# Optimization experiments

Hardware: AMD Instinct MI355X
Metric: run time of the kernel (lower is better)

Reference implementation:

```python
import jax, jax.numpy as jnp
import numpy as np

EPS = 1e-6

def _phi(u):
    # positive feature map used by linear attention
    return jax.nn.elu(u) + 1.0

def setup_inputs() -> dict:
    key = jax.random.key(0)
    ks = jax.random.split(key, 5)
    B, T, D = 8, 2048, 512  # batch, seq_len, d_model == in_features == out_features
    scale = 1.0 / np.sqrt(D)
    x = jax.random.normal(ks[0], (B, T, D), dtype=jnp.float32)
    Wq = (jax.random.normal(ks[1], (D, D), dtype=jnp.float32) * scale)
    Wk = (jax.random.normal(ks[2], (D, D), dtype=jnp.float32) * scale)
    Wv = (jax.random.normal(ks[3], (D, D), dtype=jnp.float32) * scale)
    Wp = (jax.random.normal(ks[4], (D, D), dtype=jnp.float32) * scale)  # output projection (bias=False)
    return {"x": x, "Wq": Wq, "Wk": Wk, "Wv": Wv, "Wp": Wp}

def reference(x, Wq, Wk, Wv, Wp):
    # x: [B, T, D]
    B, T, D = x.shape
    q = _phi(x @ Wq)  # [B, T, D]
    k = _phi(x @ Wk)  # [B, T, D]
    v = x @ Wv        # [B, T, D]

    # recurrent linear-attention cell, stepped over time via lax.scan
    def step(carry, qkv):
        S, z = carry              # S: [B, D, D] running sum of k^T v; z: [B, D] running sum of k
        qt, kt, vt = qkv          # each [B, D]
        S = S + kt[:, :, None] * vt[:, None, :]
        z = z + kt
        num = jnp.einsum('bd,bde->be', qt, S)        # [B, D]
        den = jnp.einsum('bd,bd->b', qt, z) + EPS    # [B]
        return (S, z), num / den[:, None]

    qT = jnp.swapaxes(q, 0, 1)  # [T, B, D]
    kT = jnp.swapaxes(k, 0, 1)
    vT = jnp.swapaxes(v, 0, 1)
    init = (jnp.zeros((B, D, D), dtype=x.dtype), jnp.zeros((B, D), dtype=x.dtype))
    _, yT = jax.lax.scan(step, init, (qT, kT, vT))  # yT: [T, B, D]
    y = jnp.swapaxes(yT, 0, 1)                      # [B, T, D]
    return y @ Wp                                   # final bias-free projection
```

## Files before the change

kernel.cpp:

```cpp
#include <hip/hip_runtime.h>


typedef __attribute__((ext_vector_type(4))) float f32x4;
typedef __attribute__((ext_vector_type(8))) __bf16 bf16x8;
typedef __attribute__((ext_vector_type(8))) unsigned short ushort8;

constexpr size_t OFF_XB  = 0;
constexpr size_t OFF_WT  = OFF_XB + 16777216;
constexpr size_t OFF_Q   = OFF_WT + 2097152;
constexpr size_t OFF_KK  = OFF_Q  + 16777216;
constexpr size_t OFF_KT  = OFF_KK + 16777216;
constexpr size_t OFF_VT  = OFF_KT + 16777216;
constexpr size_t OFF_G   = OFF_VT + 16777216;
constexpr size_t OFF_MT  = OFF_G  + 8388608;
constexpr size_t OFF_Y   = OFF_MT + 33554432;
constexpr size_t OFF_ZP  = OFF_Y  + 16777216;
constexpr size_t OFF_DEN = OFF_ZP + 131072;
constexpr size_t WS_NEED = OFF_DEN + 65536;

__device__ __forceinline__ unsigned short bfbits(float f) {
  __bf16 h = (__bf16)f;
  return __builtin_bit_cast(unsigned short, h);
}
__device__ __forceinline__ float bff(unsigned short u) {
  return (float)__builtin_bit_cast(__bf16, u);
}

__device__ __forceinline__ void gload16(const void* g, void* l) {
  __builtin_amdgcn_global_load_lds((const __attribute__((address_space(1))) void*)g,
                                   (__attribute__((address_space(3))) void*)l, 16, 0, 0);
}

__device__ __forceinline__ void stage_half(const char* gRow0, size_t ld2, int k0b,
                                           char* ldsHalf, int w, int lane) {
#pragma unroll
  for (int i = 0; i < 2; ++i) {
    int L = (w << 10) + (lane << 4) + (i << 13);
    int r = L >> 7;
    int cb = (L & 127) ^ ((r & 7) << 4);
    gload16(gRow0 + (size_t)r * ld2 + k0b + cb, ldsHalf + (w << 10) + (i << 13));
  }
}

__device__ __forceinline__ const bf16x8* frag_at(const char* halfBase, int rowInHalf,
                                                 int colByte) {
  int lin = (rowInHalf << 7) + colByte;
  lin ^= (rowInHalf & 7) << 4;
  return (const bf16x8*)(halfBase + lin);
}

#define QUAD(mh, nh)                                                                   \
  _Pragma("unroll") for (int mm = 0; mm < 4; ++mm)                                     \
  _Pragma("unroll") for (int nn = 0; nn < 2; ++nn)                                     \
  _Pragma("unroll") for (int s = 0; s < 2; ++s)                                        \
      acc[(mh)*4 + mm][(nh)*2 + nn] = __builtin_amdgcn_mfma_f32_16x16x32_bf16(         \
          af[(mh)*4 + mm][s], bg[(nh)*2 + nn][s], acc[(mh)*4 + mm][(nh)*2 + nn], 0, 0, 0);

#define PHASE_TAIL(MH, NH)                                       \
  __builtin_amdgcn_s_barrier();                                  \
  asm volatile("s_waitcnt lgkmcnt(0)" ::: "memory");             \
  __builtin_amdgcn_sched_barrier(0);                             \
  __builtin_amdgcn_s_setprio(1);                                 \
  QUAD(MH, NH);                                                  \
  __builtin_amdgcn_s_setprio(0);                                 \
  __builtin_amdgcn_s_barrier();

__device__ __forceinline__ void core8(const char* Ab, size_t lda2, const char* Bb,
                                      size_t ldb2, int nt, char* sA, char* sB,
                                      f32x4 (&acc)[8][4], int w, int lane) {
  const int mr = w >> 2, nc = w & 3;
  const int fr = lane & 15, foB = (lane >> 4) << 4;
  const int brow = (nc & 1) << 6;
  const char* gA0 = Ab;
  const char* gA1 = Ab + (size_t)128 * lda2;
  const char* gB0 = Bb;
  const char* gB1 = Bb + (size_t)128 * ldb2;
  bf16x8 af[8][2], bg[4][2];

  stage_half(gA0, lda2, 0, sA + 0 * 16384, w, lane);
  stage_half(gA1, lda2, 0, sA + 1 * 16384, w, lane);
  stage_half(gB0, ldb2, 0, sB + 0 * 16384, w, lane);
  stage_half(gB1, ldb2, 0, sB + 1 * 16384, w, lane);
  if (nt > 1) {
    stage_half(gA0, lda2, 128, sA + 2 * 16384, w, lane);
    stage_half(gA1, lda2, 128, sA + 3 * 16384, w, lane);
    asm volatile("s_waitcnt vmcnt(4)" ::: "memory");
  } else {
    asm volatile("s_waitcnt vmcnt(0)" ::: "memory");
  }
  __builtin_amdgcn_sched_barrier(0);
  __builtin_amdgcn_s_barrier();

  for (int t = 0; t < nt; ++t) {
    const int buf = t & 1;
    const char* cA = sA + buf * 32768 + mr * 16384;
    const char* cB = sB + buf * 32768 + (nc >> 1) * 16384;
    char* nA = sA + buf * 32768;
    char* nB = sB + (buf ^ 1) * 32768;
    const int kb1 = (t + 1) << 7, kb2 = (t + 2) << 7;
    const bool stB = (t + 1 < nt), stA = (t + 2 < nt);

#pragma unroll
    for (int m = 0; m < 4; ++m)
#pragma unroll
      for (int s = 0; s < 2; ++s) af[m][s] = *frag_at(cA, m * 16 + fr, s * 64 + foB);
#pragma unroll
    for (int n = 0; n < 2; ++n)
#pragma unroll
      for (int s = 0; s < 2; ++s)
        bg[n][s] = *frag_at(cB, brow + n * 16 + fr, s * 64 + foB);
    if (stB) stage_half(gB0, ldb2, kb1, nB + 0 * 16384, w, lane);
    PHASE_TAIL(0, 0)

#pragma unroll
    for (int m = 4; m < 8; ++m)
#pragma unroll
      for (int s = 0; s < 2; ++s) af[m][s] = *frag_at(cA, m * 16 + fr, s * 64 + foB);
    if (stB) stage_half(gB1, ldb2, kb1, nB + 1 * 16384, w, lane);
    PHASE_TAIL(1, 0)

#pragma unroll
    for (int n = 2; n < 4; ++n)
#pragma unroll
      for (int s = 0; s < 2; ++s)
        bg[n][s] = *frag_at(cB, brow + n * 16 + fr, s * 64 + foB);
    if (stA) stage_half(gA0, lda2, kb2, nA + 0 * 16384, w, lane);
    PHASE_TAIL(0, 1)

    if (stA) stage_half(gA1, lda2, kb2, nA + 1 * 16384, w, lane);
    if (t < nt - 2) {
      asm volatile("s_waitcnt vmcnt(4)" ::: "memory");
      __builtin_amdgcn_sched_barrier(0);
    } else if (t == nt - 2) {
      asm volatile("s_waitcnt vmcnt(0)" ::: "memory");
      __builtin_amdgcn_sched_barrier(0);
    }
    PHASE_TAIL(1, 1)
  }
}

#define QUADH(mh, nh)                                                                  \
  _Pragma("unroll") for (int mm = 0; mm < 2; ++mm)                                     \
  _Pragma("unroll") for (int nn = 0; nn < 2; ++nn)                                     \
  _Pragma("unroll") for (int s = 0; s < 2; ++s)                                        \
      acc[(mh)*2 + mm][(nh)*2 + nn] = __builtin_amdgcn_mfma_f32_16x16x32_bf16(         \
          af[(mh)*2 + mm][s], bg[(nh)*2 + nn][s], acc[(mh)*2 + mm][(nh)*2 + nn], 0, 0, 0);

#define PHASE_TAILH(MH, NH)                                      \
  __builtin_amdgcn_s_barrier();                                  \
  asm volatile("s_waitcnt lgkmcnt(0)" ::: "memory");             \
  __builtin_amdgcn_sched_barrier(0);                             \
  __builtin_amdgcn_s_setprio(1);                                 \
  QUADH(MH, NH);                                                 \
  __builtin_amdgcn_s_setprio(0);                                 \
  __builtin_amdgcn_s_barrier();

__device__ __forceinline__ void core8h(const char* Ab, size_t lda2, const char* Bb,
                                       size_t ldb2, int nt, char* sA, char* sB,
                                       f32x4 (&acc)[4][4], int w, int lane) {
  const int wr = w >> 2, wc = w & 3;
  const int fr = lane & 15, foB = (lane >> 4) << 4;
  const int brow = (wc & 1) << 6;
  const char* gB1 = Bb + (size_t)128 * ldb2;
  bf16x8 af[4][2], bg[4][2];

  stage_half(Ab, lda2, 0, sA + 0, w, lane);
  stage_half(Bb, ldb2, 0, sB + 0, w, lane);
  stage_half(gB1, ldb2, 0, sB + 16384, w, lane);
  if (nt > 1) {
    stage_half(Ab, lda2, 128, sA + 16384, w, lane);
    asm volatile("s_waitcnt vmcnt(2)" ::: "memory");
  } else {
    asm volatile("s_waitcnt vmcnt(0)" ::: "memory");
  }
  __builtin_amdgcn_sched_barrier(0);
  __builtin_amdgcn_s_barrier();

  for (int t = 0; t < nt; ++t) {
    const int buf = t & 1;
    const char* cA = sA + buf * 16384;
    const char* cB = sB + buf * 32768 + (wc >> 1) * 16384;
    char* nA = sA + buf * 16384;
    char* nB = sB + (buf ^ 1) * 32768;
    const int kb1 = (t + 1) << 7, kb2 = (t + 2) << 7;
    const bool stB = (t + 1 < nt), stA = (t + 2 < nt);

#pragma unroll
    for (int m = 0; m < 2; ++m)
#pragma unroll
      for (int s = 0; s < 2; ++s)
        af[m][s] = *frag_at(cA, wr * 64 + m * 16 + fr, s * 64 + foB);
#pragma unroll
    for (int n = 0; n < 2; ++n)
#pragma unroll
      for (int s = 0; s < 2; ++s)
        bg[n][s] = *frag_at(cB, brow + n * 16 + fr, s * 64 + foB);
    if (stB) stage_half(Bb, ldb2, kb1, nB + 0, w, lane);
    PHASE_TAILH(0, 0)

#pragma unroll
    for (int m = 2; m < 4; ++m)
#pragma unroll
      for (int s = 0; s < 2; ++s)
        af[m][s] = *frag_at(cA, wr * 64 + m * 16 + fr, s * 64 + foB);
    if (stB) stage_half(gB1, ldb2, kb1, nB + 16384, w, lane);
    PHASE_TAILH(1, 0)

#pragma unroll
    for (int n = 2; n < 4; ++n)
#pragma unroll
      for (int s = 0; s < 2; ++s)
        bg[n][s] = *frag_at(cB, brow + n * 16 + fr, s * 64 + foB);
    if (stA) stage_half(Ab, lda2, kb2, nA, w, lane);
    PHASE_TAILH(0, 1)

    if (t < nt - 1) {
      if (stA) {
        asm volatile("s_waitcnt vmcnt(2)" ::: "memory");
      } else {
        asm volatile("s_waitcnt vmcnt(0)" ::: "memory");
      }
      __builtin_amdgcn_sched_barrier(0);
    }
    PHASE_TAILH(1, 1)
  }
}

#define ACC8_INIT                                    \
  f32x4 acc[8][4];                                   \
  _Pragma("unroll") for (int m_ = 0; m_ < 8; ++m_)   \
  _Pragma("unroll") for (int n_ = 0; n_ < 4; ++n_)   \
      acc[m_][n_] = f32x4{0.f, 0.f, 0.f, 0.f};

#define ACC4_INIT                                    \
  f32x4 acc[4][4];                                   \
  _Pragma("unroll") for (int m_ = 0; m_ < 4; ++m_)   \
  _Pragma("unroll") for (int n_ = 0; n_ < 4; ++n_)   \
      acc[m_][n_] = f32x4{0.f, 0.f, 0.f, 0.f};

__global__ __launch_bounds__(512, 2) void k8_qkvt(const ushort* __restrict__ xb,
                                                  const ushort* __restrict__ wt,
                                                  ushort* __restrict__ qb,
                                                  ushort* __restrict__ kkb,
                                                  ushort* __restrict__ Kt,
                                                  ushort* __restrict__ Vt,
                                                  float* __restrict__ zsum) {
  extern __shared__ char smem[];
  const int tid = threadIdx.x, w = tid >> 6, lane = tid & 63;
  const int z = blockIdx.z, bx = blockIdx.x;
  const int at = (z < 2) ? (bx >> 1) : (bx & 1);
  const int bt = (z < 2) ? (bx & 1) : (bx >> 1);
  const ushort* wsel = wt + (z == 0 ? 0 : (z == 3 ? 524288 : 262144));
  const ushort* A = (z < 2) ? (xb + (size_t)at * 131072) : (wsel + (size_t)at * 131072);
  const ushort* Bp = (z < 2) ? (wsel + (size_t)bt * 131072) : (xb + (size_t)bt * 131072);
  ACC8_INIT
  core8((const char*)A, 1024, (const char*)Bp, 1024, 8, smem, smem + 65536, acc, w, lane);
  const int mr = w >> 2, nc = w & 3, fr = lane & 15, q4 = (lane >> 4) << 2;
  const size_t row0 = (size_t)at * 256 + mr * 128;
  const size_t col0 = (size_t)bt * 256 + nc * 64;
  if (z < 2) {
    ushort* C = z ? kkb : qb;
    float zs[4] = {0.f, 0.f, 0.f, 0.f};
#pragma unroll
    for (int m = 0; m < 8; ++m)
#pragma unroll
      for (int n = 0; n < 4; ++n)
#pragma unroll
        for (int r = 0; r < 4; ++r) {
          float v = acc[m][n][r];
          v = v > 0.f ? v + 1.f : __expf(v);
          C[(row0 + m * 16 + q4 + r) * 512 + col0 + n * 16 + fr] = bfbits(v);
          zs[n] += v;
        }
    if (z == 1) {
      float* zbuf = (float*)smem;
#pragma unroll
      for (int n = 0; n < 4; ++n) {
        zs[n] += __shfl_xor(zs[n], 16, 64);
        zs[n] += __shfl_xor(zs[n], 32, 64);
        if (lane < 16) zbuf[mr * 256 + nc * 64 + n * 16 + fr] = zs[n];
      }
      __syncthreads();
      if (tid < 256) zsum[(size_t)at * 512 + bt * 256 + tid] = zbuf[tid] + zbuf[256 + tid];
    }
  } else {
    ushort* C = (z == 2) ? Kt : Vt;
    const bool phi = (z == 2);
#pragma unroll
    for (int m = 0; m < 8; ++m)
#pragma unroll
      for (int n = 0; n < 4; ++n)
#pragma unroll
        for (int r = 0; r < 4; ++r) {
          float v = acc[m][n][r];
          if (phi) v = v > 0.f ? v + 1.f : __expf(v);
          C[(row0 + m * 16 + q4 + r) * 16384 + col0 + n * 16 + fr] = bfbits(v);
        }
  }
}

__global__ __launch_bounds__(512, 2) void k8_MG(const ushort* __restrict__ Kt,
                                                const ushort* __restrict__ Vt,
                                                const ushort* __restrict__ qb,
                                                const ushort* __restrict__ kkb,
                                                ushort* __restrict__ Mt,
                                                ushort* __restrict__ G) {
  extern __shared__ char smem[];
  const int tid = threadIdx.x, w = tid >> 6, lane = tid & 63;
  const int bx = blockIdx.x;
  if (bx < 256) {
    const int bc = bx >> 2, rt = bx & 1, ct = (bx >> 1) & 1;
    const ushort* A = Vt + (size_t)bc * 256 + (size_t)rt * 256 * 16384;
    const ushort* Bp = Kt + (size_t)bc * 256 + (size_t)ct * 256 * 16384;
    ACC8_INIT
    core8((const char*)A, 32768, (const char*)Bp, 32768, 4, smem, smem + 65536, acc, w, lane);
    ushort* C = Mt + (size_t)bc * 262144;
    const int mr = w >> 2, nc = w & 3, fr = lane & 15, q4 = (lane >> 4) << 2;
    const size_t row0 = (size_t)rt * 256 + mr * 128;
    const size_t col0 = (size_t)ct * 256 + nc * 64;
#pragma unroll
    for (int m = 0; m < 8; ++m)
#pragma unroll
      for (int n = 0; n < 4; ++n)
#pragma unroll
        for (int r = 0; r < 4; ++r)
          C[(row0 + m * 16 + q4 + r) * 512 + col0 + n * 16 + fr] = bfbits(acc[m][n][r]);
  } else {
    const int g = bx - 256;
    const int bc = g >> 1, rh = g & 1;
    const ushort* A = qb + (size_t)bc * 131072 + (size_t)rh * 65536;
    const ushort* Bp = kkb + (size_t)bc * 131072;
    ACC4_INIT
    core8h((const char*)A, 1024, (const char*)Bp, 1024, 8, smem, smem + 32768, acc, w, lane);
    ushort* Gc = G + (size_t)bc * 65536;
    const int wr = w >> 2, wc = w & 3, fr = lane & 15, q4 = (lane >> 4) << 2;
#pragma unroll
    for (int m = 0; m < 4; ++m)
#pragma unroll
      for (int n = 0; n < 4; ++n)
#pragma unroll
        for (int r = 0; r < 4; ++r) {
          int row = rh * 128 + wr * 64 + m * 16 + q4 + r;
          int col = wc * 64 + n * 16 + fr;
          float v = (col <= row) ? acc[m][n][r] : 0.f;
          Gc[(size_t)row * 256 + col] = bfbits(v);
        }
  }
}

__global__ __launch_bounds__(256) void k_dp(const ushort* __restrict__ q,
                                            const ushort* __restrict__ G,
                                            const float* __restrict__ zsum,
                                            ushort* __restrict__ Mt,
                                            float* __restrict__ den) {
  if (blockIdx.x < 4096) {
    const int l = threadIdx.x & 63;
    const int bt = blockIdx.x * 4 + (threadIdx.x >> 6);
    const int b = bt >> 11, t = bt & 2047, c = t >> 8, tl = t & 255;
    const int bc = b * 8 + c;
    const int d0 = l * 8;
    float zp[8] = {0.f, 0.f, 0.f, 0.f, 0.f, 0.f, 0.f, 0.f};
    for (int cp = 0; cp < c; ++cp) {
      const float* zr = zsum + (size_t)(b * 8 + cp) * 512 + d0;
      float4 a0 = *(const float4*)zr, a1 = *(const float4*)(zr + 4);
      zp[0] += a0.x; zp[1] += a0.y; zp[2] += a0.z; zp[3] += a0.w;
      zp[4] += a1.x; zp[5] += a1.y; zp[6] += a1.z; zp[7] += a1.w;
    }
    ushort8 qv = *(const ushort8*)&q[(size_t)bt * 512 + d0];
    float s = 0.f;
#pragma unroll
    for (int j = 0; j < 8; ++j) s = fmaf(bff(qv[j]), zp[j], s);
    const ushort* grow = G + (size_t)bc * 65536 + (size_t)tl * 256;
    const int limit = (tl & 128) ? 256 : 128;
    for (int ss = l; ss < limit; ss += 64) s += bff(grow[ss]);
#pragma unroll
    for (int off = 32; off >= 1; off >>= 1) s += __shfl_xor(s, off, 64);
    if (l == 0) den[bt] = s + 1e-6f;
  } else {
    const int g = blockIdx.x - 4096;
    const int b = g >> 7, blk = g & 127;
    ushort* base0 = Mt + (size_t)b * 8 * 262144 + (size_t)blk * 2048 + (size_t)threadIdx.x * 8;
    ushort8 mv0 = *(ushort8*)(base0 + 0 * 262144);
    ushort8 mv1 = *(ushort8*)(base0 + 1 * 262144);
    ushort8 mv2 = *(ushort8*)(base0 + 2 * 262144);
    ushort8 mv3 = *(ushort8*)(base0 + 3 * 262144);
    ushort8 mv4 = *(ushort8*)(base0 + 4 * 262144);
    ushort8 mv5 = *(ushort8*)(base0 + 5 * 262144);
    ushort8 mv6 = *(ushort8*)(base0 + 6 * 262144);
    ushort8 mv7 = *(ushort8*)(base0 + 7 * 262144);
    float a[8] = {0.f, 0.f, 0.f, 0.f, 0.f, 0.f, 0.f, 0.f};
    ushort8 ov;
#define PSTEP(c, mv)                                                     \
    _Pragma("unroll") for (int j = 0; j < 8; ++j) {                      \
      ov[j] = bfbits(a[j]); a[j] += bff(mv[j]);                          \
    }                                                                    \
    *(ushort8*)(base0 + c * 262144) = ov;
    PSTEP(0, mv0) PSTEP(1, mv1) PSTEP(2, mv2) PSTEP(3, mv3)
    PSTEP(4, mv4) PSTEP(5, mv5) PSTEP(6, mv6) PSTEP(7, mv7)
#undef PSTEP
  }
}

__global__ __launch_bounds__(512, 2) void k8_y(const ushort* __restrict__ qb,
                                               const ushort* __restrict__ G,
                                               const ushort* __restrict__ Mt,
                                               const ushort* __restrict__ Vt,
                                               const float* __restrict__ den,
                                               ushort* __restrict__ Y) {
  extern __shared__ char smem[];
  const int tid = threadIdx.x, w = tid >> 6, lane = tid & 63;
  const int rh = blockIdx.x & 1, ch = blockIdx.x >> 1, bc = blockIdx.y;
  ACC4_INIT
  core8h((const char*)(qb + (size_t)bc * 131072 + (size_t)rh * 65536), 1024,
         (const char*)(Mt + (size_t)bc * 262144 + (size_t)ch * 131072), 1024, 8,
         smem, smem + 32768, acc, w, lane);
  core8h((const char*)(G + (size_t)bc * 65536 + (size_t)rh * 32768), 512,
         (const char*)(Vt + (size_t)ch * 256 * 16384 + (size_t)bc * 256), 32768,
         rh ? 4 : 2, smem, smem + 32768, acc, w, lane);
  const int wr = w >> 2, wc = w & 3, fr = lane & 15, q4 = (lane >> 4) << 2;
#pragma unroll
  for (int m = 0; m < 4; ++m)
#pragma unroll
    for (int n = 0; n < 4; ++n)
#pragma unroll
      for (int r = 0; r < 4; ++r) {
        size_t row = (size_t)bc * 256 + rh * 128 + wr * 64 + m * 16 + q4 + r;
        size_t col = (size_t)ch * 256 + wc * 64 + n * 16 + fr;
        float v = acc[m][n][r] / den[row];
        Y[row * 512 + col] = bfbits(v);
      }
}

__global__ __launch_bounds__(512, 2) void k8_out(const ushort* __restrict__ Y,
                                                 const ushort* __restrict__ wt,
                                                 float* __restrict__ out) {
  extern __shared__ char smem[];
  const int tid = threadIdx.x, w = tid >> 6, lane = tid & 63;
  ACC4_INIT
  core8h((const char*)(Y + (size_t)blockIdx.x * 65536), 1024,
         (const char*)(wt + 786432 + (size_t)blockIdx.y * 131072), 1024, 8,
         smem, smem + 32768, acc, w, lane);
  const int wr = w >> 2, wc = w & 3, fr = lane & 15, q4 = (lane >> 4) << 2;
  const size_t row0 = (size_t)blockIdx.x * 128 + wr * 64;
  const size_t col0 = (size_t)blockIdx.y * 256 + wc * 64;
#pragma unroll
  for (int m = 0; m < 4; ++m)
#pragma unroll
    for (int n = 0; n < 4; ++n)
#pragma unroll
      for (int r = 0; r < 4; ++r)
        out[(row0 + m * 16 + q4 + r) * 512 + col0 + n * 16 + fr] = acc[m][n][r];
}

__global__ __launch_bounds__(256) void k_pre(const float* __restrict__ x,
                                             const float* __restrict__ Wq,
                                             const float* __restrict__ Wk,
                                             const float* __restrict__ Wv,
                                             const float* __restrict__ Wp,
                                             ushort* __restrict__ xb,
                                             ushort* __restrict__ wt) {
  __shared__ float tile[64][65];
  if (blockIdx.x < 4096) {
    size_t i = ((size_t)blockIdx.x * 256 + threadIdx.x) * 8;
    float4 f0 = *(const float4*)&x[i], f1 = *(const float4*)&x[i + 4];
    ushort8 o;
    o[0] = bfbits(f0.x); o[1] = bfbits(f0.y); o[2] = bfbits(f0.z); o[3] = bfbits(f0.w);
    o[4] = bfbits(f1.x); o[5] = bfbits(f1.y); o[6] = bfbits(f1.z); o[7] = bfbits(f1.w);
    *(ushort8*)&xb[i] = o;
  } else {
    const int g = blockIdx.x - 4096;
    const int bz = g >> 6, rem = g & 63, bxw = rem >> 3, byw = rem & 7;
    const float* src = bz == 0 ? Wq : bz == 1 ? Wk : bz == 2 ? Wv : Wp;
    ushort* dst = wt + (size_t)bz * 262144;
    const int d0 = bxw * 64, n0 = byw * 64;
    const int tr = threadIdx.x >> 4, tc = (threadIdx.x & 15) << 2;
#pragma unroll
    for (int it = 0; it < 4; ++it) {
      float4 f = *(const float4*)&src[(size_t)(d0 + it * 16 + tr) * 512 + n0 + tc];
      tile[it * 16 + tr][tc + 0] = f.x;
      tile[it * 16 + tr][tc + 1] = f.y;
      tile[it * 16 + tr][tc + 2] = f.z;
      tile[it * 16 + tr][tc + 3] = f.w;
    }
    __syncthreads();
#pragma unroll
    for (int it = 0; it < 4; ++it) {
      int n = it * 16 + tr;
      ushort4 o;
      o.x = bfbits(tile[tc + 0][n]);
      o.y = bfbits(tile[tc + 1][n]);
      o.z = bfbits(tile[tc + 2][n]);
      o.w = bfbits(tile[tc + 3][n]);
      *(ushort4*)&dst[(size_t)(n0 + n) * 512 + d0 + tc] = o;
    }
  }
}

extern "C" void kernel_launch(void* const* d_in, const int* in_sizes, int n_in,
                              void* d_out, int out_size, void* d_ws, size_t ws_size,
                              hipStream_t stream) {
  const float* x  = (const float*)d_in[0];
  const float* Wq = (const float*)d_in[1];
  const float* Wk = (const float*)d_in[2];
  const float* Wv = (const float*)d_in[3];
  const float* Wp = (const float*)d_in[4];
  float* out = (float*)d_out;
  char* ws8 = (char*)d_ws;
  if (ws_size < WS_NEED) return;

  ushort* xb  = (ushort*)(ws8 + OFF_XB);
  ushort* wt  = (ushort*)(ws8 + OFF_WT);
  ushort* qb  = (ushort*)(ws8 + OFF_Q);
  ushort* kkb = (ushort*)(ws8 + OFF_KK);
  ushort* Kt  = (ushort*)(ws8 + OFF_KT);
  ushort* Vt  = (ushort*)(ws8 + OFF_VT);
  ushort* G   = (ushort*)(ws8 + OFF_G);
  ushort* Mt  = (ushort*)(ws8 + OFF_MT);
  ushort* Y   = (ushort*)(ws8 + OFF_Y);
  float*  zp  = (float*)(ws8 + OFF_ZP);
  float*  den = (float*)(ws8 + OFF_DEN);

  constexpr int SMEM_BIG = 131072, SMEM_H = 98304;
  hipFuncSetAttribute((const void*)k8_qkvt, hipFuncAttributeMaxDynamicSharedMemorySize, SMEM_BIG);
  hipFuncSetAttribute((const void*)k8_MG,   hipFuncAttributeMaxDynamicSharedMemorySize, SMEM_BIG);
  hipFuncSetAttribute((const void*)k8_y,    hipFuncAttributeMaxDynamicSharedMemorySize, SMEM_H);
  hipFuncSetAttribute((const void*)k8_out,  hipFuncAttributeMaxDynamicSharedMemorySize, SMEM_H);

  k_pre<<<4352, 256, 0, stream>>>(x, Wq, Wk, Wv, Wp, xb, wt);
  k8_qkvt<<<dim3(128, 1, 4), 512, SMEM_BIG, stream>>>(xb, wt, qb, kkb, Kt, Vt, zp);
  k8_MG<<<384, 512, SMEM_BIG, stream>>>(Kt, Vt, qb, kkb, Mt, G);
  k_dp<<<5120, 256, 0, stream>>>(qb, G, zp, Mt, den);
  k8_y<<<dim3(4, 64), 512, SMEM_H, stream>>>(qb, G, Mt, Vt, den, Y);
  k8_out<<<dim3(128, 2), 512, SMEM_H, stream>>>(Y, wt, out);
}
```

Baseline: 155.6 us.

## Compute K once for both layouts and fold denominator into MG kernel

The QKV projection kernel now runs three GEMM slices (Q, K, V) on 128x256 tiles instead of four (Q, K, K-transposed, V-transposed). The K tile is written both row-major and transposed, and V goes straight to the transposed layout with vectorized stores, which removes one redundant x@Wk GEMM. The denominator computation is moved into the G branch of the MG kernel, using row sums of the masked G and a prefix of per-half zsum partials. The Mt prefix scan becomes its own small kernel. This trades redundant GEMM work and a separate den pass for strided transposed stores and more epilogue work in the MG kernel.

```diff
diff --git a/kernel.cpp b/kernel.cpp
--- a/kernel.cpp
+++ b/kernel.cpp
@@ -15,7 +15,7 @@
 constexpr size_t OFF_MT  = OFF_G  + 8388608;
 constexpr size_t OFF_Y   = OFF_MT + 33554432;
 constexpr size_t OFF_ZP  = OFF_Y  + 16777216;
-constexpr size_t OFF_DEN = OFF_ZP + 131072;
+constexpr size_t OFF_DEN = OFF_ZP + 262144;
 constexpr size_t WS_NEED = OFF_DEN + 65536;
 
 __device__ __forceinline__ unsigned short bfbits(float f) {
@@ -244,58 +244,72 @@
                                                   ushort* __restrict__ kkb,
                                                   ushort* __restrict__ Kt,
                                                   ushort* __restrict__ Vt,
-                                                  float* __restrict__ zsum) {
+                                                  float* __restrict__ zsumH) {
   extern __shared__ char smem[];
   const int tid = threadIdx.x, w = tid >> 6, lane = tid & 63;
-  const int z = blockIdx.z, bx = blockIdx.x;
-  const int at = (z < 2) ? (bx >> 1) : (bx & 1);
-  const int bt = (z < 2) ? (bx & 1) : (bx >> 1);
-  const ushort* wsel = wt + (z == 0 ? 0 : (z == 3 ? 524288 : 262144));
-  const ushort* A = (z < 2) ? (xb + (size_t)at * 131072) : (wsel + (size_t)at * 131072);
-  const ushort* Bp = (z < 2) ? (wsel + (size_t)bt * 131072) : (xb + (size_t)bt * 131072);
-  ACC8_INIT
-  core8((const char*)A, 1024, (const char*)Bp, 1024, 8, smem, smem + 65536, acc, w, lane);
-  const int mr = w >> 2, nc = w & 3, fr = lane & 15, q4 = (lane >> 4) << 2;
-  const size_t row0 = (size_t)at * 256 + mr * 128;
-  const size_t col0 = (size_t)bt * 256 + nc * 64;
-  if (z < 2) {
-    ushort* C = z ? kkb : qb;
-    float zs[4] = {0.f, 0.f, 0.f, 0.f};
-#pragma unroll
-    for (int m = 0; m < 8; ++m)
+  const int z = blockIdx.z, mt = blockIdx.x, ct = blockIdx.y;
+  const ushort* wsel = wt + (z == 0 ? 0 : (z == 1 ? 262144 : 524288));
+  const ushort* A = xb + (size_t)mt * 128 * 512;
+  const ushort* Bp = wsel + (size_t)ct * 256 * 512;
+  ACC4_INIT
+  core8h((const char*)A, 1024, (const char*)Bp, 1024, 8, smem, smem + 32768, acc, w, lane);
+  const int wr = w >> 2, wc = w & 3, fr = lane & 15, q4 = (lane >> 4) << 2;
+  const size_t row0 = (size_t)mt * 128 + wr * 64;
+  const size_t col0 = (size_t)ct * 256 + wc * 64;
+  if (z == 0) {
+#pragma unroll
+    for (int m = 0; m < 4; ++m)
 #pragma unroll
       for (int n = 0; n < 4; ++n)
 #pragma unroll
         for (int r = 0; r < 4; ++r) {
           float v = acc[m][n][r];
           v = v > 0.f ? v + 1.f : __expf(v);
-          C[(row0 + m * 16 + q4 + r) * 512 + col0 + n * 16 + fr] = bfbits(v);
-          zs[n] += v;
+          qb[(row0 + m * 16 + q4 + r) * 512 + col0 + n * 16 + fr] = bfbits(v);
         }
-    if (z == 1) {
-      float* zbuf = (float*)smem;
+  } else if (z == 2) {
+#pragma unroll
+    for (int m = 0; m < 4; ++m)
 #pragma unroll
       for (int n = 0; n < 4; ++n) {
-        zs[n] += __shfl_xor(zs[n], 16, 64);
-        zs[n] += __shfl_xor(zs[n], 32, 64);
-        if (lane < 16) zbuf[mr * 256 + nc * 64 + n * 16 + fr] = zs[n];
+        ushort4 o;
+        o.x = bfbits(acc[m][n][0]);
+        o.y = bfbits(acc[m][n][1]);
+        o.z = bfbits(acc[m][n][2]);
+        o.w = bfbits(acc[m][n][3]);
+        *(ushort4*)&Vt[(col0 + n * 16 + fr) * 16384 + row0 + m * 16 + q4] = o;
       }
-      __syncthreads();
-      if (tid < 256) zsum[(size_t)at * 512 + bt * 256 + tid] = zbuf[tid] + zbuf[256 + tid];
-    }
   } else {
-    ushort* C = (z == 2) ? Kt : Vt;
-    const bool phi = (z == 2);
-#pragma unroll
-    for (int m = 0; m < 8; ++m)
-#pragma unroll
-      for (int n = 0; n < 4; ++n)
+    float zs[4] = {0.f, 0.f, 0.f, 0.f};
+#pragma unroll
+    for (int m = 0; m < 4; ++m)
+#pragma unroll
+      for (int n = 0; n < 4; ++n) {
+        float ph[4];
 #pragma unroll
         for (int r = 0; r < 4; ++r) {
           float v = acc[m][n][r];
-          if (phi) v = v > 0.f ? v + 1.f : __expf(v);
-          C[(row0 + m * 16 + q4 + r) * 16384 + col0 + n * 16 + fr] = bfbits(v);
+          ph[r] = v > 0.f ? v + 1.f : __expf(v);
+          kkb[(row0 + m * 16 + q4 + r) * 512 + col0 + n * 16 + fr] = bfbits(ph[r]);
+          zs[n] += ph[r];
         }
+        ushort4 o;
+        o.x = bfbits(ph[0]); o.y = bfbits(ph[1]); o.z = bfbits(ph[2]); o.w = bfbits(ph[3]);
+        *(ushort4*)&Kt[(col0 + n * 16 + fr) * 16384 + row0 + m * 16 + q4] = o;
+      }
+#pragma unroll
+    for (int n = 0; n < 4; ++n) {
+      zs[n] += __shfl_xor(zs[n], 16, 64);
+      zs[n] += __shfl_xor(zs[n], 32, 64);
+    }
+    float* zbuf = (float*)smem;
+    if (lane < 16) {
+#pragma unroll
+      for (int n = 0; n < 4; ++n) zbuf[wr * 256 + wc * 64 + n * 16 + fr] = zs[n];
+    }
+    __syncthreads();
+    if (tid < 256)
+      zsumH[(size_t)mt * 512 + ct * 256 + tid] = zbuf[tid] + zbuf[256 + tid];
   }
 }
 
@@ -303,21 +317,23 @@
                                                 const ushort* __restrict__ Vt,
                                                 const ushort* __restrict__ qb,
                                                 const ushort* __restrict__ kkb,
+                                                const float* __restrict__ zsumH,
                                                 ushort* __restrict__ Mt,
-                                                ushort* __restrict__ G) {
+                                                ushort* __restrict__ G,
+                                                float* __restrict__ den) {
   extern __shared__ char smem[];
   const int tid = threadIdx.x, w = tid >> 6, lane = tid & 63;
   const int bx = blockIdx.x;
   if (bx < 256) {
-    const int bc = bx >> 2, rt = bx & 1, ct = (bx >> 1) & 1;
+    const int bc = bx >> 2, rt = bx & 1, ctl = (bx >> 1) & 1;
     const ushort* A = Vt + (size_t)bc * 256 + (size_t)rt * 256 * 16384;
-    const ushort* Bp = Kt + (size_t)bc * 256 + (size_t)ct * 256 * 16384;
+    const ushort* Bp = Kt + (size_t)bc * 256 + (size_t)ctl * 256 * 16384;
     ACC8_INIT
     core8((const char*)A, 32768, (const char*)Bp, 32768, 4, smem, smem + 65536, acc, w, lane);
     ushort* C = Mt + (size_t)bc * 262144;
     const int mr = w >> 2, nc = w & 3, fr = lane & 15, q4 = (lane >> 4) << 2;
     const size_t row0 = (size_t)rt * 256 + mr * 128;
-    const size_t col0 = (size_t)ct * 256 + nc * 64;
+    const size_t col0 = (size_t)ctl * 256 + nc * 64;
 #pragma unroll
     for (int m = 0; m < 8; ++m)
 #pragma unroll
@@ -328,12 +344,18 @@
   } else {
     const int g = bx - 256;
     const int bc = g >> 1, rh = g & 1;
+    const int b = bc >> 3, c = bc & 7;
     const ushort* A = qb + (size_t)bc * 131072 + (size_t)rh * 65536;
     const ushort* Bp = kkb + (size_t)bc * 131072;
     ACC4_INIT
     core8h((const char*)A, 1024, (const char*)Bp, 1024, 8, smem, smem + 32768, acc, w, lane);
     ushort* Gc = G + (size_t)bc * 65536;
     const int wr = w >> 2, wc = w & 3, fr = lane & 15, q4 = (lane >> 4) << 2;
+    float rs[4][4];
+#pragma unroll
+    for (int m = 0; m < 4; ++m)
+#pragma unroll
+      for (int r = 0; r < 4; ++r) rs[m][r] = 0.f;
 #pragma unroll
     for (int m = 0; m < 4; ++m)
 #pragma unroll
@@ -344,61 +366,75 @@
           int col = wc * 64 + n * 16 + fr;
           float v = (col <= row) ? acc[m][n][r] : 0.f;
           Gc[(size_t)row * 256 + col] = bfbits(v);
+          rs[m][r] += v;
         }
-  }
-}
-
-__global__ __launch_bounds__(256) void k_dp(const ushort* __restrict__ q,
-                                            const ushort* __restrict__ G,
-                                            const float* __restrict__ zsum,
-                                            ushort* __restrict__ Mt,
-                                            float* __restrict__ den) {
-  if (blockIdx.x < 4096) {
-    const int l = threadIdx.x & 63;
-    const int bt = blockIdx.x * 4 + (threadIdx.x >> 6);
-    const int b = bt >> 11, t = bt & 2047, c = t >> 8, tl = t & 255;
-    const int bc = b * 8 + c;
-    const int d0 = l * 8;
-    float zp[8] = {0.f, 0.f, 0.f, 0.f, 0.f, 0.f, 0.f, 0.f};
-    for (int cp = 0; cp < c; ++cp) {
-      const float* zr = zsum + (size_t)(b * 8 + cp) * 512 + d0;
-      float4 a0 = *(const float4*)zr, a1 = *(const float4*)(zr + 4);
-      zp[0] += a0.x; zp[1] += a0.y; zp[2] += a0.z; zp[3] += a0.w;
-      zp[4] += a1.x; zp[5] += a1.y; zp[6] += a1.z; zp[7] += a1.w;
-    }
-    ushort8 qv = *(const ushort8*)&q[(size_t)bt * 512 + d0];
-    float s = 0.f;
-#pragma unroll
-    for (int j = 0; j < 8; ++j) s = fmaf(bff(qv[j]), zp[j], s);
-    const ushort* grow = G + (size_t)bc * 65536 + (size_t)tl * 256;
-    const int limit = (tl & 128) ? 256 : 128;
-    for (int ss = l; ss < limit; ss += 64) s += bff(grow[ss]);
-#pragma unroll
-    for (int off = 32; off >= 1; off >>= 1) s += __shfl_xor(s, off, 64);
-    if (l == 0) den[bt] = s + 1e-6f;
-  } else {
-    const int g = blockIdx.x - 4096;
-    const int b = g >> 7, blk = g & 127;
-    ushort* base0 = Mt + (size_t)b * 8 * 262144 + (size_t)blk * 2048 + (size_t)threadIdx.x * 8;
-    ushort8 mv0 = *(ushort8*)(base0 + 0 * 262144);
-    ushort8 mv1 = *(ushort8*)(base0 + 1 * 262144);
-    ushort8 mv2 = *(ushort8*)(base0 + 2 * 262144);
-    ushort8 mv3 = *(ushort8*)(base0 + 3 * 262144);
-    ushort8 mv4 = *(ushort8*)(base0 + 4 * 262144);
-    ushort8 mv5 = *(ushort8*)(base0 + 5 * 262144);
-    ushort8 mv6 = *(ushort8*)(base0 + 6 * 262144);
-    ushort8 mv7 = *(ushort8*)(base0 + 7 * 262144);
-    float a[8] = {0.f, 0.f, 0.f, 0.f, 0.f, 0.f, 0.f, 0.f};
-    ushort8 ov;
-#define PSTEP(c, mv)                                                     \
-    _Pragma("unroll") for (int j = 0; j < 8; ++j) {                      \
-      ov[j] = bfbits(a[j]); a[j] += bff(mv[j]);                          \
-    }                                                                    \
-    *(ushort8*)(base0 + c * 262144) = ov;
-    PSTEP(0, mv0) PSTEP(1, mv1) PSTEP(2, mv2) PSTEP(3, mv3)
-    PSTEP(4, mv4) PSTEP(5, mv5) PSTEP(6, mv6) PSTEP(7, mv7)
+#pragma unroll
+    for (int m = 0; m < 4; ++m)
+#pragma unroll
+      for (int r = 0; r < 4; ++r) {
+        rs[m][r] += __shfl_xor(rs[m][r], 1, 64);
+        rs[m][r] += __shfl_xor(rs[m][r], 2, 64);
+        rs[m][r] += __shfl_xor(rs[m][r], 4, 64);
+        rs[m][r] += __shfl_xor(rs[m][r], 8, 64);
+      }
+    float* red = (float*)smem;
+    float* zpl = red + 512;
+    if (fr == 0) {
+      int rbase = wr * 64 + q4;
+#pragma unroll
+      for (int m = 0; m < 4; ++m)
+#pragma unroll
+        for (int r = 0; r < 4; ++r) red[wc * 128 + rbase + m * 16 + r] = rs[m][r];
+    }
+    {
+      float a = 0.f;
+      for (int cp = 0; cp < c; ++cp)
+        a += zsumH[(size_t)((b * 8 + cp) * 2) * 512 + tid] +
+             zsumH[(size_t)((b * 8 + cp) * 2 + 1) * 512 + tid];
+      zpl[tid] = a;
+    }
+    __syncthreads();
+    {
+      int rl = tid >> 2, quarter = tid & 3;
+      int trow = bc * 256 + rh * 128 + rl;
+      const ushort* qrow = qb + (size_t)trow * 512 + quarter * 128;
+      const float* zq = zpl + quarter * 128;
+      float s = 0.f;
+      for (int j = 0; j < 128; j += 8) {
+        ushort8 qv = *(const ushort8*)&qrow[j];
+#pragma unroll
+        for (int u = 0; u < 8; ++u) s = fmaf(bff(qv[u]), zq[j + u], s);
+      }
+      s += __shfl_xor(s, 1, 64);
+      s += __shfl_xor(s, 2, 64);
+      if (quarter == 0)
+        den[trow] = s + red[rl] + red[128 + rl] + red[256 + rl] + red[384 + rl] + 1e-6f;
+    }
+  }
+}
+
+__global__ __launch_bounds__(256) void k_prefix(ushort* __restrict__ Mt) {
+  const int g = blockIdx.x;
+  const int b = g >> 7, blk = g & 127;
+  ushort* base0 = Mt + (size_t)b * 8 * 262144 + (size_t)blk * 2048 + (size_t)threadIdx.x * 8;
+  ushort8 mv0 = *(ushort8*)(base0 + 0 * 262144);
+  ushort8 mv1 = *(ushort8*)(base0 + 1 * 262144);
+  ushort8 mv2 = *(ushort8*)(base0 + 2 * 262144);
+  ushort8 mv3 = *(ushort8*)(base0 + 3 * 262144);
+  ushort8 mv4 = *(ushort8*)(base0 + 4 * 262144);
+  ushort8 mv5 = *(ushort8*)(base0 + 5 * 262144);
+  ushort8 mv6 = *(ushort8*)(base0 + 6 * 262144);
+  ushort8 mv7 = *(ushort8*)(base0 + 7 * 262144);
+  float a[8] = {0.f, 0.f, 0.f, 0.f, 0.f, 0.f, 0.f, 0.f};
+  ushort8 ov;
+#define PSTEP(c, mv)                                                   \
+  _Pragma("unroll") for (int j = 0; j < 8; ++j) {                      \
+    ov[j] = bfbits(a[j]); a[j] += bff(mv[j]);                          \
+  }                                                                    \
+  *(ushort8*)(base0 + c * 262144) = ov;
+  PSTEP(0, mv0) PSTEP(1, mv1) PSTEP(2, mv2) PSTEP(3, mv3)
+  PSTEP(4, mv4) PSTEP(5, mv5) PSTEP(6, mv6) PSTEP(7, mv7)
 #undef PSTEP
-  }
 }
 
 __global__ __launch_bounds__(512, 2) void k8_y(const ushort* __restrict__ qb,
@@ -517,19 +553,19 @@
   ushort* G   = (ushort*)(ws8 + OFF_G);
   ushort* Mt  = (ushort*)(ws8 + OFF_MT);
   ushort* Y   = (ushort*)(ws8 + OFF_Y);
-  float*  zp  = (float*)(ws8 + OFF_ZP);
+  float*  zpH = (float*)(ws8 + OFF_ZP);
   float*  den = (float*)(ws8 + OFF_DEN);
 
   constexpr int SMEM_BIG = 131072, SMEM_H = 98304;
-  hipFuncSetAttribute((const void*)k8_qkvt, hipFuncAttributeMaxDynamicSharedMemorySize, SMEM_BIG);
+  hipFuncSetAttribute((const void*)k8_qkvt, hipFuncAttributeMaxDynamicSharedMemorySize, SMEM_H);
   hipFuncSetAttribute((const void*)k8_MG,   hipFuncAttributeMaxDynamicSharedMemorySize, SMEM_BIG);
   hipFuncSetAttribute((const void*)k8_y,    hipFuncAttributeMaxDynamicSharedMemorySize, SMEM_H);
   hipFuncSetAttribute((const void*)k8_out,  hipFuncAttributeMaxDynamicSharedMemorySize, SMEM_H);
 
   k_pre<<<4352, 256, 0, stream>>>(x, Wq, Wk, Wv, Wp, xb, wt);
-  k8_qkvt<<<dim3(128, 1, 4), 512, SMEM_BIG, stream>>>(xb, wt, qb, kkb, Kt, Vt, zp);
-  k8_MG<<<384, 512, SMEM_BIG, stream>>>(Kt, Vt, qb, kkb, Mt, G);
-  k_dp<<<5120, 256, 0, stream>>>(qb, G, zp, Mt, den);
+  k8_qkvt<<<dim3(128, 2, 3), 512, SMEM_H, stream>>>(xb, wt, qb, kkb, Kt, Vt, zpH);
+  k8_MG<<<384, 512, SMEM_BIG, stream>>>(Kt, Vt, qb, kkb, zpH, Mt, G, den);
+  k_prefix<<<1024, 256, 0, stream>>>(Mt);
   k8_y<<<dim3(4, 64), 512, SMEM_H, stream>>>(qb, G, Mt, Vt, den, Y);
   k8_out<<<dim3(128, 2), 512, SMEM_H, stream>>>(Y, wt, out);
 }
```

After: 144.9 us. 6.9% less time.
